# Kernel optimization log

Hardware: AMD Instinct MI355X
Metric: run time of the kernel (lower is better)

## Reference

```python
import jax, jax.numpy as jnp
import numpy as np

N = 4096
DIM = 128      # dim_in
HID = 256      # mlp hidden_dim
K_IN = 8       # k for linear_k

def _knn_edges(dist, k):
    # dist: [n,n]; k nearest neighbors excluding self (matches heapq loop)
    n = dist.shape[0]
    d = jnp.where(jnp.eye(n, dtype=bool), jnp.inf, dist)
    nbr = jax.lax.top_k(-d, k)[1]                     # [n,k] indices of k smallest
    src = jnp.repeat(jnp.arange(n), k)                # res[0] = i
    dst = nbr.reshape(-1)                             # res[1] = neighbor
    return src, dst

def _gcn_conv(x, src, dst, W, b):
    # torch_geometric GCNConv: add self loops + symmetric normalization
    n = x.shape[0]
    loop = jnp.arange(n)
    s = jnp.concatenate([src, loop])
    t = jnp.concatenate([dst, loop])
    xw = x @ W
    deg = jax.ops.segment_sum(jnp.ones(s.shape[0], x.dtype), t, num_segments=n)
    dinv = jax.lax.rsqrt(deg)                         # deg >= 1 due to self loops
    norm = dinv[s] * dinv[t]
    out = jax.ops.segment_sum(norm[:, None] * xw[s], t, num_segments=n)
    return out + b

def _gcn(x, src, dst, Wg1, bg1, Wg2, bg2):
    h = jax.nn.relu(_gcn_conv(x, src, dst, Wg1, bg1))
    h = _gcn_conv(h, src, dst, Wg2, bg2)              # dropout is identity in eval
    return jax.nn.log_softmax(h, axis=1)

def _conv2d(x, w, b):
    y = jax.lax.conv_general_dilated(x, w, (1, 1), 'SAME',
        dimension_numbers=('NCHW', 'OIHW', 'NCHW'))
    return y + b.reshape(1, -1, 1, 1)

def setup_inputs():
    key = jax.random.key(0)
    ks = jax.random.split(key, 20)
    f32 = jnp.float32
    def w(k, shape):
        fan = shape[0]
        return (jax.random.uniform(k, shape, f32) * 2 - 1) * (1.0 / np.sqrt(fan))
    return {
        'data_x_1': jax.random.normal(ks[0], (1, N, 4), f32),
        'data_x_2': jax.random.normal(ks[1], (1, N, K_IN, 4), f32),
        'Wk': w(ks[2], (K_IN, 1)),        'bk': jnp.zeros((1,), f32),
        'Wg1': w(ks[3], (8, DIM // 2)),   'bg1': jnp.zeros((DIM // 2,), f32),
        'Wg2': w(ks[4], (DIM // 2, DIM)), 'bg2': jnp.zeros((DIM,), f32),
        'Wq': w(ks[5], (3 * DIM, DIM)),   'bq': jnp.zeros((DIM,), f32),
        'Wkey': w(ks[6], (3 * DIM, DIM)), 'bkey': jnp.zeros((DIM,), f32),
        'Woff': w(ks[7], (4, DIM)),       'boff': jnp.zeros((DIM,), f32),
        'pw': jnp.full((1,), 0.25, f32),
        'Wf1': w(ks[8], (DIM, HID)),      'bf1': jnp.zeros((HID,), f32),
        'Wf2': w(ks[9], (HID, HID)),      'bf2': jnp.zeros((HID,), f32),
        'Wf3': w(ks[10], (HID, 4)),       'bf3': jnp.zeros((4,), f32),
        'Wcy3': w(ks[11], (1, 1, 1, 3)),  'bcy3': jnp.zeros((1,), f32),
        'Wcx3': w(ks[12], (1, 1, 3, 1)),  'bcx3': jnp.zeros((1,), f32),
        'Wcy5': w(ks[13], (1, 1, 1, 5)),  'bcy5': jnp.zeros((1,), f32),
        'Wcx5': w(ks[14], (1, 1, 5, 1)),  'bcx5': jnp.zeros((1,), f32),
        'Wcy9': w(ks[15], (1, 1, 1, 9)),  'bcy9': jnp.zeros((1,), f32),
        'Wcx9': w(ks[16], (1, 1, 9, 1)),  'bcx9': jnp.zeros((1,), f32),
    }

def reference(data_x_1, data_x_2, Wk, bk, Wg1, bg1, Wg2, bg2, Wq, bq, Wkey, bkey,
              Woff, boff, pw, Wf1, bf1, Wf2, bf2, Wf3, bf3,
              Wcy3, bcy3, Wcx3, bcx3, Wcy5, bcy5, Wcx5, bcx5, Wcy9, bcy9, Wcx9, bcx9):
    # linear_k over k dimension: [1,n,k,4] -> transpose -> [1,n,4,k] -> [1,n,4]
    dx2 = jnp.swapaxes(data_x_2, 2, 3)
    dx2_out = (dx2 @ Wk + bk)[..., 0]
    data_x = jnp.concatenate([data_x_1, dx2_out], axis=2)   # [1,n,8]
    Ot = data_x[:, :, 4:]                                   # [1,n,4]

    pos = data_x[:, :, 0:2]
    diff = pos[:, :, None, :] - pos[:, None, :, :]          # [1,n,n,2]
    distances = jnp.linalg.norm(diff, axis=3)               # [1,n,n]
    maxd = jnp.max(distances, axis=2, keepdims=True)
    oushi_atte = 1.0 - distances / maxd                     # [1,n,n]

    x0 = data_x[0]
    dist0 = jax.lax.stop_gradient(distances[0])             # knn on detached dist
    embs = []
    for kk in (3, 5, 9):
        src, dst = _knn_edges(dist0, kk)
        embs.append(_gcn(x0, src, dst, Wg1, bg1, Wg2, bg2)[None])
    embedding = jnp.concatenate(embs, axis=2)               # [1,n,3*DIM]

    query = embedding @ Wq + bq                             # [1,n,DIM]
    key_t = embedding @ Wkey + bkey
    scores = jnp.einsum('bnd,bmd->bnm', query, key_t) / jnp.sqrt(jnp.float32(DIM))
    A = scores / jnp.max(scores, axis=2, keepdims=True)     # [1,n,n]

    A4 = A[None]                                            # [1,1,n,n]
    c3 = _conv2d(A4, Wcy3, bcy3) + _conv2d(A4, Wcx3, bcx3)
    c5 = _conv2d(A4, Wcy5, bcy5) + _conv2d(A4, Wcx5, bcx5)
    c9 = _conv2d(A4, Wcy9, bcy9) + _conv2d(A4, Wcx9, bcx9)

    A_cat = jnp.concatenate([A, oushi_atte, c3[0], c5[0], c9[0]], axis=2)  # [1,n,5n]
    A_cat = (A_cat - A_cat.min()) / (A_cat.max() - A_cat.min())

    Ot5 = jnp.tile(Ot, (1, 5, 1))                           # [1,5n,4]
    h = jnp.matmul(A_cat, Ot5)                              # [1,n,4]
    h = h @ Woff + boff                                     # [1,n,DIM]
    h = jnp.where(h > 0, h, pw * h)                         # PReLU (scalar weight)
    h = jax.nn.relu(h @ Wf1 + bf1)
    h = jax.nn.relu(h @ Wf2 + bf2)
    return h @ Wf3 + bf3                                    # [1,n,4]
```

## Files before the change

kernel.cpp:

```cpp
#include <hip/hip_runtime.h>
#include <math.h>

#define NN 4096

static __device__ __forceinline__ unsigned enc_f(float f){
    unsigned u = __float_as_uint(f);
    return (u & 0x80000000u) ? ~u : (u | 0x80000000u);
}
static __device__ __forceinline__ float dec_f(unsigned u){
    unsigned b = (u & 0x80000000u) ? (u & 0x7fffffffu) : ~u;
    return __uint_as_float(b);
}

__global__ void k_prep(const float* __restrict__ dx1, const float* __restrict__ dx2,
                       const float* __restrict__ Wk, const float* __restrict__ bk,
                       float* __restrict__ x0, float* __restrict__ colsum){
    int n = blockIdx.x*blockDim.x + threadIdx.x;
    if (n >= NN) return;
    float wk[8];
    #pragma unroll
    for (int j=0;j<8;j++) wk[j] = Wk[j];
    float bkv = bk[0];
    #pragma unroll
    for (int c=0;c<4;c++) x0[n*8+c] = dx1[n*4+c];
    #pragma unroll
    for (int c=0;c<4;c++){
        float acc = bkv;
        #pragma unroll
        for (int j=0;j<8;j++) acc += dx2[(n*8+j)*4+c]*wk[j];
        x0[n*8+4+c] = acc;
        atomicAdd(&colsum[c], acc);
    }
}

__global__ __launch_bounds__(256) void k_dist(const float* __restrict__ dx1,
        float* __restrict__ maxd, int* __restrict__ nbr,
        int* __restrict__ cnt3, int* __restrict__ cnt5, int* __restrict__ cnt9){
    __shared__ float2 ps[NN];
    int tid = threadIdx.x;
    for (int j=tid; j<NN; j+=256){
        float4 v = *(const float4*)&dx1[j*4];
        ps[j] = make_float2(v.x, v.y);
    }
    __syncthreads();
    int lane = tid & 63;
    int i = blockIdx.x*4 + (tid>>6);
    float2 pi = ps[i];
    unsigned long long best[9];
    #pragma unroll
    for (int q=0;q<9;q++) best[q] = ~0ULL;
    float lmax = 0.f;
    for (int t=0;t<64;t++){
        int j = (t<<6) | lane;
        float2 p = ps[j];
        float dx = pi.x - p.x, dy = pi.y - p.y;
        float d = sqrtf(dx*dx + dy*dy);
        lmax = fmaxf(lmax, d);
        unsigned long long cand = ((unsigned long long)__float_as_uint(d) << 32) | (unsigned)j;
        if (j != i && cand < best[8]){
            best[8] = cand;
            #pragma unroll
            for (int q=8; q>0; --q){
                if (best[q] < best[q-1]){ unsigned long long tm=best[q]; best[q]=best[q-1]; best[q-1]=tm; }
            }
        }
    }
    #pragma unroll
    for (int m=1;m<64;m<<=1) lmax = fmaxf(lmax, __shfl_xor(lmax, m, 64));
    if (lane==0) maxd[i] = lmax;
    for (int t=0;t<9;t++){
        unsigned long long w = best[0];
        #pragma unroll
        for (int m=1;m<64;m<<=1){
            unsigned long long o = __shfl_xor(w, m, 64);
            if (o < w) w = o;
        }
        if (best[0] == w){
            #pragma unroll
            for (int q=0;q<8;q++) best[q] = best[q+1];
            best[8] = ~0ULL;
        }
        if (lane==0){
            int j = (int)(w & 0xffffffffu);
            nbr[i*9+t] = j;
            atomicAdd(&cnt9[j], 1);
            if (t<5) atomicAdd(&cnt5[j], 1);
            if (t<3) atomicAdd(&cnt3[j], 1);
        }
    }
}

__global__ __launch_bounds__(256) void k_scan(const int* __restrict__ cnt3,
        const int* __restrict__ cnt5, const int* __restrict__ cnt9,
        int* __restrict__ offc, float* __restrict__ dinvc){
    __shared__ int part[256];
    int tid = threadIdx.x;
    for (int g=0; g<3; g++){
        const int* cp = g==0?cnt3:(g==1?cnt5:cnt9);
        int base = tid*16;
        int loc[16]; int s=0;
        #pragma unroll
        for (int q=0;q<16;q++){ loc[q]=s; s += cp[base+q]; }
        part[tid]=s; __syncthreads();
        for (int d=1; d<256; d<<=1){
            int v = (tid>=d) ? part[tid-d] : 0;
            __syncthreads();
            part[tid] += v;
            __syncthreads();
        }
        int pre = (tid==0) ? 0 : part[tid-1];
        #pragma unroll
        for (int q=0;q<16;q++){
            offc[g*NN + base + q]  = pre + loc[q];
            dinvc[g*NN + base + q] = rsqrtf((float)cp[base+q] + 1.f);
        }
        __syncthreads();
    }
}

__global__ void k_fill(const int* __restrict__ nbr, const int* __restrict__ offc,
        int* __restrict__ cur, int* __restrict__ rev){
    int i = blockIdx.x*256 + threadIdx.x;
    if (i >= NN) return;
    #pragma unroll
    for (int t=0;t<9;t++){
        int j = nbr[i*9+t];
        int gmin = t<3 ? 0 : (t<5 ? 1 : 2);
        for (int g=gmin; g<3; g++){
            int pos = atomicAdd(&cur[g*NN+j], 1);
            int rb = (g==0) ? 0 : (g==1 ? NN*3 : NN*8);
            rev[rb + offc[g*NN+j] + pos] = i;
        }
    }
}

__global__ void k_y1(const float* __restrict__ x0, const float* __restrict__ Wg1,
                     float* __restrict__ xw){
    int idx = blockIdx.x*256 + threadIdx.x;
    if (idx >= NN*64) return;
    int n = idx>>6, c = idx&63;
    float acc = 0.f;
    #pragma unroll
    for (int k=0;k<8;k++) acc += x0[n*8+k]*Wg1[k*64+c];
    xw[idx] = acc;
}

__global__ __launch_bounds__(256) void k_h1y2(const float* __restrict__ xw,
        const int* __restrict__ offc,
        const int* __restrict__ cnt3, const int* __restrict__ cnt5, const int* __restrict__ cnt9,
        const int* __restrict__ rev, const float* __restrict__ dinvc,
        const float* __restrict__ bg1, const float* __restrict__ Wg2,
        float* __restrict__ y2){
    __shared__ float h1s[12][64];
    int n0 = blockIdx.x*4, tid = threadIdx.x;
    for (int s=tid; s<768; s+=256){
        int p = s>>6, k = s&63, g = p>>2, n = n0+(p&3);
        const int* cp = g==0?cnt3:(g==1?cnt5:cnt9);
        int rb = (g==0) ? 0 : (g==1 ? NN*3 : NN*8);
        int cnt = cp[n];
        int o = rb + offc[g*NN+n];
        float dv = dinvc[g*NN+n];
        float srow = dv*xw[n*64+k];
        for (int e=0;e<cnt;e++){
            int i = rev[o+e];
            srow += dinvc[g*NN+i]*xw[i*64+k];
        }
        float v = dv*srow + bg1[k];
        h1s[p][k] = v>0.f ? v : 0.f;
    }
    __syncthreads();
    int c = tid & 127, ph = tid>>7;
    float a6[6] = {0,0,0,0,0,0};
    for (int k=0;k<64;k++){
        float w = Wg2[k*128+c];
        #pragma unroll
        for (int q=0;q<6;q++) a6[q] += h1s[q*2+ph][k]*w;
    }
    #pragma unroll
    for (int q=0;q<6;q++){
        int p = q*2+ph, g = p>>2, n = n0+(p&3);
        float dv = dinvc[g*NN+n];
        y2[(size_t)g*NN*128 + (size_t)n*128 + c] = dv*a6[q];
    }
}

__global__ __launch_bounds__(128) void k_fin(const float* __restrict__ y2,
        const int* __restrict__ offc,
        const int* __restrict__ cnt3, const int* __restrict__ cnt5, const int* __restrict__ cnt9,
        const int* __restrict__ rev, const float* __restrict__ dinvc,
        const float* __restrict__ bg2, float* __restrict__ emb){
    __shared__ float sm[2], ss[2];
    int b = blockIdx.x;
    int n = b & (NN-1), g = b >> 12;
    const int* cp = g==0?cnt3:(g==1?cnt5:cnt9);
    int rb = (g==0) ? 0 : (g==1 ? NN*3 : NN*8);
    int cnt = cp[n];
    int o = rb + offc[g*NN+n];
    float dv = dinvc[g*NN+n];
    int c = threadIdx.x;
    const float* yg = y2 + (size_t)g*NN*128;
    float s = yg[(size_t)n*128 + c];
    for (int e=0;e<cnt;e++){
        int i = rev[o+e];
        s += yg[(size_t)i*128 + c];
    }
    float v = dv*s + bg2[c];
    float m = v;
    #pragma unroll
    for (int st=1;st<64;st<<=1) m = fmaxf(m, __shfl_xor(m, st, 64));
    if ((c&63)==0) sm[c>>6] = m;
    __syncthreads();
    m = fmaxf(sm[0], sm[1]);
    float e = expf(v - m);
    float t = e;
    #pragma unroll
    for (int st=1;st<64;st<<=1) t += __shfl_xor(t, st, 64);
    if ((c&63)==0) ss[c>>6] = t;
    __syncthreads();
    t = ss[0]+ss[1];
    emb[n*384 + g*128 + c] = v - m - logf(t);
}

__global__ __launch_bounds__(256) void k_qk(const float* __restrict__ emb,
        const float* __restrict__ Wq, const float* __restrict__ bq,
        const float* __restrict__ Wkey, const float* __restrict__ bkey,
        float* __restrict__ q, float* __restrict__ kbuf){
    __shared__ float es[8][384];
    int n0 = blockIdx.x*8;
    int tid = threadIdx.x;
    for (int idx=tid; idx<8*384; idx+=256){
        int m = idx/384, k = idx%384;
        es[m][k] = emb[(n0+m)*384+k];
    }
    __syncthreads();
    int c = tid & 127;
    int sel = tid >> 7;
    const float* W = sel ? Wkey : Wq;
    float b = sel ? bkey[c] : bq[c];
    float acc[8];
    #pragma unroll
    for (int m=0;m<8;m++) acc[m]=b;
    for (int k=0;k<384;k++){
        float w = W[k*128+c];
        #pragma unroll
        for (int m=0;m<8;m++) acc[m] += es[m][k]*w;
    }
    float* out = sel ? kbuf : q;
    #pragma unroll
    for (int m=0;m<8;m++) out[(n0+m)*128+c] = acc[m];
}

__global__ __launch_bounds__(256) void k_scores(const float* __restrict__ q,
        const float* __restrict__ kb, float* __restrict__ scores,
        unsigned* __restrict__ rowmaxenc){
    __shared__ float at[32][132];
    __shared__ float bt[32][132];
    int bx = blockIdx.x & 31;
    int by = blockIdx.x >> 5;
    int r0 = by*128, c0 = bx*128;
    int tid = threadIdx.x;
    int tx = tid & 15, ty = tid >> 4;
    float acc[8][8] = {};
    for (int k0 = 0; k0 < 128; k0 += 32){
        __syncthreads();
        #pragma unroll
        for (int l=0; l<4; l++){
            int idx = tid + l*256;
            int rowi = idx >> 3;
            int kq  = (idx & 7) * 4;
            float4 a = *(const float4*)&q [(size_t)(r0+rowi)*128 + k0 + kq];
            float4 b = *(const float4*)&kb[(size_t)(c0+rowi)*128 + k0 + kq];
            at[kq+0][rowi]=a.x; at[kq+1][rowi]=a.y; at[kq+2][rowi]=a.z; at[kq+3][rowi]=a.w;
            bt[kq+0][rowi]=b.x; bt[kq+1][rowi]=b.y; bt[kq+2][rowi]=b.z; bt[kq+3][rowi]=b.w;
        }
        __syncthreads();
        #pragma unroll
        for (int k=0;k<32;k++){
            float4 a0 = *(const float4*)&at[k][ty*4];
            float4 a1 = *(const float4*)&at[k][64+ty*4];
            float4 b0 = *(const float4*)&bt[k][tx*4];
            float4 b1 = *(const float4*)&bt[k][64+tx*4];
            float av[8] = {a0.x,a0.y,a0.z,a0.w,a1.x,a1.y,a1.z,a1.w};
            float bv[8] = {b0.x,b0.y,b0.z,b0.w,b1.x,b1.y,b1.z,b1.w};
            #pragma unroll
            for (int u=0;u<8;u++){
                #pragma unroll
                for (int v=0;v<8;v++) acc[u][v] += av[u]*bv[v];
            }
        }
    }
    #pragma unroll
    for (int u=0;u<8;u++){
        int rr = r0 + ((u<4)? ty*4+u : 64+ty*4+(u-4));
        float4 s0 = {acc[u][0],acc[u][1],acc[u][2],acc[u][3]};
        float4 s1 = {acc[u][4],acc[u][5],acc[u][6],acc[u][7]};
        *(float4*)&scores[(size_t)rr*NN + c0 + tx*4] = s0;
        *(float4*)&scores[(size_t)rr*NN + c0 + 64 + tx*4] = s1;
        float m = acc[u][0];
        #pragma unroll
        for (int v=1;v<8;v++) m = fmaxf(m, acc[u][v]);
        #pragma unroll
        for (int s=1;s<16;s<<=1) m = fmaxf(m, __shfl_xor(m, s, 64));
        if (tx==0) atomicMax(&rowmaxenc[rr], enc_f(m));
    }
}

__global__ __launch_bounds__(256) void k_mcat(const float* __restrict__ scores,
        const unsigned* __restrict__ rowmaxenc, const float* __restrict__ maxd,
        const float* __restrict__ dx1, const float* __restrict__ x0,
        const float* __restrict__ Wcy3, const float* __restrict__ Wcx3,
        const float* __restrict__ Wcy5, const float* __restrict__ Wcx5,
        const float* __restrict__ Wcy9, const float* __restrict__ Wcx9,
        const float* __restrict__ bcy3, const float* __restrict__ bcx3,
        const float* __restrict__ bcy5, const float* __restrict__ bcx5,
        const float* __restrict__ bcy9, const float* __restrict__ bcx9,
        float* __restrict__ mnmx, float* __restrict__ hpart){
    __shared__ float As[40][76];
    __shared__ float invr[40];
    __shared__ float2 pj[64];
    __shared__ float4 ots[64];
    __shared__ float2 pi[32];
    __shared__ float im[32];
    __shared__ float smn[256], smx[256];
    int xb = blockIdx.x, yb = blockIdx.y;
    int i0 = yb*32, j0 = xb*64;
    int tid = threadIdx.x;
    float wy3[3],wx3[3],wy5[5],wx5[5],wy9[9],wx9[9];
    #pragma unroll
    for (int t=0;t<3;t++){ wy3[t]=Wcy3[t]; wx3[t]=Wcx3[t]; }
    #pragma unroll
    for (int t=0;t<5;t++){ wy5[t]=Wcy5[t]; wx5[t]=Wcx5[t]; }
    #pragma unroll
    for (int t=0;t<9;t++){ wy9[t]=Wcy9[t]; wx9[t]=Wcx9[t]; }
    float bc3 = bcy3[0]+bcx3[0];
    float bc5 = bcy5[0]+bcx5[0];
    float bc9 = bcy9[0]+bcx9[0];
    if (tid < 40){
        int gr = i0-4+tid;
        invr[tid] = ((unsigned)gr < NN) ? 1.f/dec_f(rowmaxenc[gr]) : 0.f;
    } else if (tid >= 64 && tid < 128){
        int c = tid-64, j = j0+c;
        float4 v = *(const float4*)&dx1[j*4];
        pj[c] = make_float2(v.x, v.y);
        ots[c] = *(const float4*)&x0[j*8+4];
    } else if (tid >= 128 && tid < 160){
        int r = tid-128;
        float4 v = *(const float4*)&dx1[(i0+r)*4];
        pi[r] = make_float2(v.x, v.y);
        im[r] = 1.f/maxd[i0+r];
    }
    __syncthreads();
    for (int idx=tid; idx<40*72; idx+=256){
        int lr = idx/72, lc = idx - lr*72;
        int gr = i0-4+lr, gc = j0-4+lc;
        float v = 0.f;
        if ((unsigned)gr < NN && (unsigned)gc < NN)
            v = scores[(size_t)gr*NN + gc]*invr[lr];
        As[lr][lc] = v;
    }
    __syncthreads();
    int r = tid>>3, cb = tid&7, c0l = cb*8;
    float acc9[8]={0,0,0,0,0,0,0,0}, acc5[8]={0,0,0,0,0,0,0,0}, acc3[8]={0,0,0,0,0,0,0,0}, ctr[8];
    #pragma unroll
    for (int u=0;u<9;u++){
        float4 a = *(const float4*)&As[r+u][c0l+4];
        float4 b = *(const float4*)&As[r+u][c0l+8];
        float vals[8] = {a.x,a.y,a.z,a.w,b.x,b.y,b.z,b.w};
        #pragma unroll
        for (int q=0;q<8;q++){
            acc9[q] += vals[q]*wx9[u];
            if (u>=2 && u<=6) acc5[q] += vals[q]*wx5[u-2];
            if (u>=3 && u<=5) acc3[q] += vals[q]*wx3[u-3];
            if (u==4) ctr[q] = vals[q];
        }
    }
    float win[16];
    #pragma unroll
    for (int q4=0;q4<4;q4++){
        float4 w4 = *(const float4*)&As[r+4][c0l+q4*4];
        win[q4*4+0]=w4.x; win[q4*4+1]=w4.y; win[q4*4+2]=w4.z; win[q4*4+3]=w4.w;
    }
    float mn = INFINITY, mx = -INFINITY;
    float pd0=0,pd1=0,pd2=0,pd3=0;
    float2 ppi = pi[r];
    float imv = im[r];
    #pragma unroll
    for (int q=0;q<8;q++){
        float cy9=0.f;
        #pragma unroll
        for (int u=0;u<9;u++) cy9 += win[q+u]*wy9[u];
        float cy5=0.f;
        #pragma unroll
        for (int u=0;u<5;u++) cy5 += win[q+2+u]*wy5[u];
        float cy3=0.f;
        #pragma unroll
        for (int u=0;u<3;u++) cy3 += win[q+3+u]*wy3[u];
        float c3v = cy3+acc3[q]+bc3;
        float c5v = cy5+acc5[q]+bc5;
        float c9v = cy9+acc9[q]+bc9;
        float a = ctr[q];
        float2 pjv = pj[c0l+q];
        float dxp = ppi.x-pjv.x, dyp = ppi.y-pjv.y;
        float ou = 1.f - sqrtf(dxp*dxp+dyp*dyp)*imv;
        float Mv = a + ou + c3v + c5v + c9v;
        mn = fminf(mn, fminf(fminf(a,ou), fminf(fminf(c3v,c5v),c9v)));
        mx = fmaxf(mx, fmaxf(fmaxf(a,ou), fmaxf(fmaxf(c3v,c5v),c9v)));
        float4 ot = ots[c0l+q];
        pd0 += Mv*ot.x; pd1 += Mv*ot.y; pd2 += Mv*ot.z; pd3 += Mv*ot.w;
    }
    #pragma unroll
    for (int m=1;m<8;m<<=1){
        pd0 += __shfl_xor(pd0, m, 64);
        pd1 += __shfl_xor(pd1, m, 64);
        pd2 += __shfl_xor(pd2, m, 64);
        pd3 += __shfl_xor(pd3, m, 64);
    }
    if (cb==0){
        float4 pd = {pd0,pd1,pd2,pd3};
        *(float4*)&hpart[((size_t)(i0+r)*64 + xb)*4] = pd;
    }
    smn[tid]=mn; smx[tid]=mx; __syncthreads();
    for (int s=128;s>0;s>>=1){
        if (tid<s){ smn[tid]=fminf(smn[tid],smn[tid+s]); smx[tid]=fmaxf(smx[tid],smx[tid+s]); }
        __syncthreads();
    }
    if (tid==0){
        int bid = yb*64 + xb;
        mnmx[bid] = smn[0];
        mnmx[8192 + bid] = smx[0];
    }
}

__global__ __launch_bounds__(256) void k_gmm(const float* __restrict__ mnmx, float* __restrict__ gmm){
    __shared__ float smn[256], smx[256];
    int tid = threadIdx.x;
    float mn = INFINITY, mx = -INFINITY;
    for (int i=tid; i<8192; i+=256){
        mn = fminf(mn, mnmx[i]);
        mx = fmaxf(mx, mnmx[8192+i]);
    }
    smn[tid]=mn; smx[tid]=mx; __syncthreads();
    for (int s=128;s>0;s>>=1){
        if (tid<s){ smn[tid]=fminf(smn[tid],smn[tid+s]); smx[tid]=fmaxf(smx[tid],smx[tid+s]); }
        __syncthreads();
    }
    if (tid==0){ gmm[0]=smn[0]; gmm[1]=smx[0]; }
}

__global__ __launch_bounds__(256) void k_hred(const float* __restrict__ hpart,
        const float* __restrict__ gmm, const float* __restrict__ colsum,
        float* __restrict__ hfin){
    int i = blockIdx.x*256 + threadIdx.x;
    if (i >= NN) return;
    float4 sum = {0,0,0,0};
    const float4* hp = (const float4*)hpart + (size_t)i*64;
    for (int xb=0; xb<64; xb++){
        float4 v = hp[xb];
        sum.x+=v.x; sum.y+=v.y; sum.z+=v.z; sum.w+=v.w;
    }
    float mnv = gmm[0], mxv = gmm[1];
    float s = 1.f/(mxv-mnv), o = -mnv*s;
    float4 cs = *(const float4*)colsum;
    float4 out;
    out.x = s*sum.x + 5.f*o*cs.x;
    out.y = s*sum.y + 5.f*o*cs.y;
    out.z = s*sum.z + 5.f*o*cs.z;
    out.w = s*sum.w + 5.f*o*cs.w;
    *(float4*)&hfin[i*4] = out;
}

__global__ __launch_bounds__(256) void k_mlp(const float* __restrict__ hfin,
        const float* __restrict__ Woff, const float* __restrict__ boff, const float* __restrict__ pw,
        const float* __restrict__ Wf1, const float* __restrict__ bf1,
        const float* __restrict__ Wf2, const float* __restrict__ bf2,
        const float* __restrict__ Wf3, const float* __restrict__ bf3,
        float* __restrict__ out){
    __shared__ float h1[8][128];
    __shared__ float h2[8][256];
    __shared__ float h3[8][256];
    __shared__ float4 red4[256];
    int n0 = blockIdx.x*8, tid = threadIdx.x;
    float p = pw[0];
    {
        int c = tid & 127, mb = (tid>>7)*4;
        #pragma unroll
        for (int mm=0; mm<4; mm++){
            int m = mb+mm;
            float v = boff[c];
            #pragma unroll
            for (int k=0;k<4;k++) v += hfin[(n0+m)*4+k]*Woff[k*128+c];
            h1[m][c] = v>0.f ? v : p*v;
        }
    }
    __syncthreads();
    {
        int c = tid;
        float acc[8];
        #pragma unroll
        for (int m=0;m<8;m++) acc[m] = bf1[c];
        for (int k=0;k<128;k++){
            float w = Wf1[k*256+c];
            #pragma unroll
            for (int m=0;m<8;m++) acc[m] += h1[m][k]*w;
        }
        #pragma unroll
        for (int m=0;m<8;m++) h2[m][c] = acc[m]>0.f?acc[m]:0.f;
    }
    __syncthreads();
    {
        int c = tid;
        float acc[8];
        #pragma unroll
        for (int m=0;m<8;m++) acc[m] = bf2[c];
        for (int k=0;k<256;k++){
            float w = Wf2[k*256+c];
            #pragma unroll
            for (int m=0;m<8;m++) acc[m] += h2[m][k]*w;
        }
        #pragma unroll
        for (int m=0;m<8;m++) h3[m][c] = acc[m]>0.f?acc[m]:0.f;
    }
    __syncthreads();
    float w3_0 = Wf3[tid*4+0], w3_1 = Wf3[tid*4+1], w3_2 = Wf3[tid*4+2], w3_3 = Wf3[tid*4+3];
    for (int m=0;m<8;m++){
        float hv = h3[m][tid];
        float4 r; r.x = hv*w3_0; r.y = hv*w3_1; r.z = hv*w3_2; r.w = hv*w3_3;
        red4[tid]=r; __syncthreads();
        for (int s=128;s>0;s>>=1){
            if(tid<s){
                red4[tid].x+=red4[tid+s].x; red4[tid].y+=red4[tid+s].y;
                red4[tid].z+=red4[tid+s].z; red4[tid].w+=red4[tid+s].w;
            }
            __syncthreads();
        }
        if (tid==0){
            float4 o;
            o.x = red4[0].x + bf3[0]; o.y = red4[0].y + bf3[1];
            o.z = red4[0].z + bf3[2]; o.w = red4[0].w + bf3[3];
            *(float4*)&out[(n0+m)*4] = o;
        }
        __syncthreads();
    }
}

extern "C" void kernel_launch(void* const* d_in, const int* in_sizes, int n_in,
                              void* d_out, int out_size, void* d_ws, size_t ws_size,
                              hipStream_t stream){
    const float* dx1  = (const float*)d_in[0];
    const float* dx2  = (const float*)d_in[1];
    const float* Wk   = (const float*)d_in[2];
    const float* bk   = (const float*)d_in[3];
    const float* Wg1  = (const float*)d_in[4];
    const float* bg1  = (const float*)d_in[5];
    const float* Wg2  = (const float*)d_in[6];
    const float* bg2  = (const float*)d_in[7];
    const float* Wq   = (const float*)d_in[8];
    const float* bq   = (const float*)d_in[9];
    const float* Wkey = (const float*)d_in[10];
    const float* bkey = (const float*)d_in[11];
    const float* Woff = (const float*)d_in[12];
    const float* boff = (const float*)d_in[13];
    const float* pw   = (const float*)d_in[14];
    const float* Wf1  = (const float*)d_in[15];
    const float* bf1  = (const float*)d_in[16];
    const float* Wf2  = (const float*)d_in[17];
    const float* bf2  = (const float*)d_in[18];
    const float* Wf3  = (const float*)d_in[19];
    const float* bf3  = (const float*)d_in[20];
    const float* Wcy3 = (const float*)d_in[21];
    const float* bcy3 = (const float*)d_in[22];
    const float* Wcx3 = (const float*)d_in[23];
    const float* bcx3 = (const float*)d_in[24];
    const float* Wcy5 = (const float*)d_in[25];
    const float* bcy5 = (const float*)d_in[26];
    const float* Wcx5 = (const float*)d_in[27];
    const float* bcx5 = (const float*)d_in[28];
    const float* Wcy9 = (const float*)d_in[29];
    const float* bcy9 = (const float*)d_in[30];
    const float* Wcx9 = (const float*)d_in[31];
    const float* bcx9 = (const float*)d_in[32];

    char* ws = (char*)d_ws;
    size_t off = 0;
    auto alloc = [&](size_t b)->void*{ void* p = ws + off; off += (b + 255) & ~(size_t)255; return p; };

    char* zbase = ws + off;
    float*    colsum    = (float*)   alloc(4*4);
    int*      cnt3      = (int*)     alloc((size_t)NN*4);
    int*      cnt5      = (int*)     alloc((size_t)NN*4);
    int*      cnt9      = (int*)     alloc((size_t)NN*4);
    int*      cur       = (int*)     alloc((size_t)3*NN*4);
    unsigned* rowmaxenc = (unsigned*)alloc((size_t)NN*4);
    size_t zbytes = (size_t)((ws + off) - zbase);

    float* x0     = (float*)alloc((size_t)NN*8*4);
    float* maxd   = (float*)alloc((size_t)NN*4);
    int*   nbr    = (int*)  alloc((size_t)NN*9*4);
    int*   offc   = (int*)  alloc((size_t)3*NN*4);
    float* dinvc  = (float*)alloc((size_t)3*NN*4);
    int*   rev    = (int*)  alloc((size_t)NN*17*4);
    float* xw     = (float*)alloc((size_t)NN*64*4);
    float* y2     = (float*)alloc((size_t)3*NN*128*4);
    float* emb    = (float*)alloc((size_t)NN*384*4);
    float* qb     = (float*)alloc((size_t)NN*128*4);
    float* kb     = (float*)alloc((size_t)NN*128*4);
    float* scores = (float*)alloc((size_t)NN*NN*4);
    float* mnmx   = (float*)alloc((size_t)2*8192*4);
    float* hpart  = (float*)alloc((size_t)NN*64*4*4);
    float* gmm    = (float*)alloc(2*4);
    float* hfin   = (float*)alloc((size_t)NN*4*4);
    (void)ws_size; (void)in_sizes; (void)n_in; (void)out_size;

    hipMemsetAsync(zbase, 0, zbytes, stream);

    k_prep<<<16,256,0,stream>>>(dx1,dx2,Wk,bk,x0,colsum);
    k_dist<<<NN/4,256,0,stream>>>(dx1,maxd,nbr,cnt3,cnt5,cnt9);
    k_scan<<<1,256,0,stream>>>(cnt3,cnt5,cnt9,offc,dinvc);
    k_fill<<<16,256,0,stream>>>(nbr,offc,cur,rev);

    k_y1  <<<NN*64/256,256,0,stream>>>(x0,Wg1,xw);
    k_h1y2<<<NN/4,256,0,stream>>>(xw,offc,cnt3,cnt5,cnt9,rev,dinvc,bg1,Wg2,y2);
    k_fin <<<NN*3,128,0,stream>>>(y2,offc,cnt3,cnt5,cnt9,rev,dinvc,bg2,emb);

    k_qk<<<NN/8,256,0,stream>>>(emb,Wq,bq,Wkey,bkey,qb,kb);
    k_scores<<<1024,256,0,stream>>>(qb,kb,scores,rowmaxenc);
    k_mcat<<<dim3(64,128),256,0,stream>>>(scores,rowmaxenc,maxd,dx1,x0,
        Wcy3,Wcx3,Wcy5,Wcx5,Wcy9,Wcx9,
        bcy3,bcx3,bcy5,bcx5,bcy9,bcx9, mnmx, hpart);
    k_gmm<<<1,256,0,stream>>>(mnmx,gmm);
    k_hred<<<NN/256,256,0,stream>>>(hpart,gmm,colsum,hfin);
    k_mlp<<<NN/8,256,0,stream>>>(hfin,Woff,boff,pw,Wf1,bf1,Wf2,bf2,Wf3,bf3,(float*)d_out);
}
```

Measured before the change: 354.7 us.

## Enlarge mcat tiles, vectorize swizzled score loads, move A min/max into scores

The fused conv/concat kernel now works on 64x64 tiles instead of 32x64. This cuts the share of halo rows re-read from the large scores matrix. Tiles are loaded as float4 into an XOR-swizzled shared-memory layout, each thread computes two output rows, and the block min/max uses wave shuffles instead of a 256-entry shared tree. The per-row min of the scores is now gathered with atomics in the scores kernel, so the global normalization bounds for A and the oushi term come from row min/max (oushi assumed to span [0,1]). This costs an extra atomicMin per row segment and an extra memset.

```diff
diff --git a/kernel.cpp b/kernel.cpp
--- a/kernel.cpp
+++ b/kernel.cpp
@@ -252,7 +252,7 @@
 
 __global__ __launch_bounds__(256) void k_scores(const float* __restrict__ q,
         const float* __restrict__ kb, float* __restrict__ scores,
-        unsigned* __restrict__ rowmaxenc){
+        unsigned* __restrict__ rowmaxenc, unsigned* __restrict__ rowminenc){
     __shared__ float at[32][132];
     __shared__ float bt[32][132];
     int bx = blockIdx.x & 31;
@@ -296,12 +296,18 @@
         float4 s1 = {acc[u][4],acc[u][5],acc[u][6],acc[u][7]};
         *(float4*)&scores[(size_t)rr*NN + c0 + tx*4] = s0;
         *(float4*)&scores[(size_t)rr*NN + c0 + 64 + tx*4] = s1;
-        float m = acc[u][0];
-        #pragma unroll
-        for (int v=1;v<8;v++) m = fmaxf(m, acc[u][v]);
-        #pragma unroll
-        for (int s=1;s<16;s<<=1) m = fmaxf(m, __shfl_xor(m, s, 64));
-        if (tx==0) atomicMax(&rowmaxenc[rr], enc_f(m));
+        float m = acc[u][0], mn = acc[u][0];
+        #pragma unroll
+        for (int v=1;v<8;v++){ m = fmaxf(m, acc[u][v]); mn = fminf(mn, acc[u][v]); }
+        #pragma unroll
+        for (int s=1;s<16;s<<=1){
+            m  = fmaxf(m,  __shfl_xor(m,  s, 64));
+            mn = fminf(mn, __shfl_xor(mn, s, 64));
+        }
+        if (tx==0){
+            atomicMax(&rowmaxenc[rr], enc_f(m));
+            atomicMin(&rowminenc[rr], enc_f(mn));
+        }
     }
 }
 
@@ -315,16 +321,17 @@
         const float* __restrict__ bcy5, const float* __restrict__ bcx5,
         const float* __restrict__ bcy9, const float* __restrict__ bcx9,
         float* __restrict__ mnmx, float* __restrict__ hpart){
-    __shared__ float As[40][76];
-    __shared__ float invr[40];
-    __shared__ float2 pj[64];
+    __shared__ float As[72][96];
+    __shared__ float invr_s[72];
     __shared__ float4 ots[64];
-    __shared__ float2 pi[32];
-    __shared__ float im[32];
-    __shared__ float smn[256], smx[256];
-    int xb = blockIdx.x, yb = blockIdx.y;
-    int i0 = yb*32, j0 = xb*64;
+    __shared__ float2 pjv[64];
+    __shared__ float2 piv[64];
+    __shared__ float ims[64];
+    __shared__ float smn[4], smx[4];
+    int bx = blockIdx.x, by = blockIdx.y;
+    int i0 = by*64, j0 = bx*64;
     int tid = threadIdx.x;
+
     float wy3[3],wx3[3],wy5[5],wx5[5],wy9[9],wx9[9];
     #pragma unroll
     for (int t=0;t<3;t++){ wy3[t]=Wcy3[t]; wx3[t]=Wcx3[t]; }
@@ -335,109 +342,157 @@
     float bc3 = bcy3[0]+bcx3[0];
     float bc5 = bcy5[0]+bcx5[0];
     float bc9 = bcy9[0]+bcx9[0];
-    if (tid < 40){
+
+    if (tid < 72){
         int gr = i0-4+tid;
-        invr[tid] = ((unsigned)gr < NN) ? 1.f/dec_f(rowmaxenc[gr]) : 0.f;
-    } else if (tid >= 64 && tid < 128){
-        int c = tid-64, j = j0+c;
+        invr_s[tid] = ((unsigned)gr < NN) ? 1.f/dec_f(rowmaxenc[gr]) : 0.f;
+    } else if (tid >= 96 && tid < 160){
+        int c = tid-96, j = j0+c;
         float4 v = *(const float4*)&dx1[j*4];
-        pj[c] = make_float2(v.x, v.y);
+        pjv[c] = make_float2(v.x, v.y);
         ots[c] = *(const float4*)&x0[j*8+4];
-    } else if (tid >= 128 && tid < 160){
-        int r = tid-128;
+    } else if (tid >= 160 && tid < 224){
+        int r = tid-160;
         float4 v = *(const float4*)&dx1[(i0+r)*4];
-        pi[r] = make_float2(v.x, v.y);
-        im[r] = 1.f/maxd[i0+r];
-    }
-    __syncthreads();
-    for (int idx=tid; idx<40*72; idx+=256){
-        int lr = idx/72, lc = idx - lr*72;
-        int gr = i0-4+lr, gc = j0-4+lc;
-        float v = 0.f;
-        if ((unsigned)gr < NN && (unsigned)gc < NN)
-            v = scores[(size_t)gr*NN + gc]*invr[lr];
-        As[lr][lc] = v;
-    }
-    __syncthreads();
-    int r = tid>>3, cb = tid&7, c0l = cb*8;
-    float acc9[8]={0,0,0,0,0,0,0,0}, acc5[8]={0,0,0,0,0,0,0,0}, acc3[8]={0,0,0,0,0,0,0,0}, ctr[8];
-    #pragma unroll
-    for (int u=0;u<9;u++){
-        float4 a = *(const float4*)&As[r+u][c0l+4];
-        float4 b = *(const float4*)&As[r+u][c0l+8];
-        float vals[8] = {a.x,a.y,a.z,a.w,b.x,b.y,b.z,b.w};
-        #pragma unroll
-        for (int q=0;q<8;q++){
-            acc9[q] += vals[q]*wx9[u];
-            if (u>=2 && u<=6) acc5[q] += vals[q]*wx5[u-2];
-            if (u>=3 && u<=5) acc3[q] += vals[q]*wx3[u-3];
-            if (u==4) ctr[q] = vals[q];
-        }
-    }
-    float win[16];
-    #pragma unroll
-    for (int q4=0;q4<4;q4++){
-        float4 w4 = *(const float4*)&As[r+4][c0l+q4*4];
-        win[q4*4+0]=w4.x; win[q4*4+1]=w4.y; win[q4*4+2]=w4.z; win[q4*4+3]=w4.w;
-    }
+        piv[r] = make_float2(v.x, v.y);
+        ims[r] = 1.f/maxd[i0+r];
+    }
+    __syncthreads();
+
+    bool colEdge = (bx == 0) || (bx == 63);
+    for (int s = tid; s < 72*20; s += 256){
+        int row = s/20, c4 = s - row*20;
+        int gr = i0 - 4 + row;
+        int grc = gr < 0 ? 0 : (gr > NN-1 ? NN-1 : gr);
+        int gcf = j0 - 8 + c4*4;
+        float iv = invr_s[row];
+        float4 v;
+        if (!colEdge){
+            v = *(const float4*)&scores[(size_t)grc*NN + gcf];
+        } else {
+            v = make_float4(0.f,0.f,0.f,0.f);
+            const float* rp = &scores[(size_t)grc*NN];
+            if ((unsigned)(gcf+0) < NN) v.x = rp[gcf+0];
+            if ((unsigned)(gcf+1) < NN) v.y = rp[gcf+1];
+            if ((unsigned)(gcf+2) < NN) v.z = rp[gcf+2];
+            if ((unsigned)(gcf+3) < NN) v.w = rp[gcf+3];
+        }
+        int sc4 = c4 ^ ((row & 3) << 1);
+        float* dst = &As[row][sc4*4];
+        dst[0]=v.x*iv; dst[1]=v.y*iv; dst[2]=v.z*iv; dst[3]=v.w*iv;
+    }
+    __syncthreads();
+
+    int rp = tid >> 3, cg = tid & 7;
+    int r0l = rp*2;
     float mn = INFINITY, mx = -INFINITY;
-    float pd0=0,pd1=0,pd2=0,pd3=0;
-    float2 ppi = pi[r];
-    float imv = im[r];
-    #pragma unroll
-    for (int q=0;q<8;q++){
-        float cy9=0.f;
-        #pragma unroll
-        for (int u=0;u<9;u++) cy9 += win[q+u]*wy9[u];
-        float cy5=0.f;
-        #pragma unroll
-        for (int u=0;u<5;u++) cy5 += win[q+2+u]*wy5[u];
-        float cy3=0.f;
-        #pragma unroll
-        for (int u=0;u<3;u++) cy3 += win[q+3+u]*wy3[u];
-        float c3v = cy3+acc3[q]+bc3;
-        float c5v = cy5+acc5[q]+bc5;
-        float c9v = cy9+acc9[q]+bc9;
-        float a = ctr[q];
-        float2 pjv = pj[c0l+q];
-        float dxp = ppi.x-pjv.x, dyp = ppi.y-pjv.y;
-        float ou = 1.f - sqrtf(dxp*dxp+dyp*dyp)*imv;
-        float Mv = a + ou + c3v + c5v + c9v;
-        mn = fminf(mn, fminf(fminf(a,ou), fminf(fminf(c3v,c5v),c9v)));
-        mx = fmaxf(mx, fmaxf(fmaxf(a,ou), fmaxf(fmaxf(c3v,c5v),c9v)));
-        float4 ot = ots[c0l+q];
-        pd0 += Mv*ot.x; pd1 += Mv*ot.y; pd2 += Mv*ot.z; pd3 += Mv*ot.w;
-    }
-    #pragma unroll
-    for (int m=1;m<8;m<<=1){
-        pd0 += __shfl_xor(pd0, m, 64);
-        pd1 += __shfl_xor(pd1, m, 64);
-        pd2 += __shfl_xor(pd2, m, 64);
-        pd3 += __shfl_xor(pd3, m, 64);
-    }
-    if (cb==0){
-        float4 pd = {pd0,pd1,pd2,pd3};
-        *(float4*)&hpart[((size_t)(i0+r)*64 + xb)*4] = pd;
-    }
-    smn[tid]=mn; smx[tid]=mx; __syncthreads();
-    for (int s=128;s>0;s>>=1){
-        if (tid<s){ smn[tid]=fminf(smn[tid],smn[tid+s]); smx[tid]=fmaxf(smx[tid],smx[tid+s]); }
-        __syncthreads();
-    }
-    if (tid==0){
-        int bid = yb*64 + xb;
-        mnmx[bid] = smn[0];
-        mnmx[8192 + bid] = smx[0];
-    }
-}
-
-__global__ __launch_bounds__(256) void k_gmm(const float* __restrict__ mnmx, float* __restrict__ gmm){
+    float pdx[2]={0,0}, pdy[2]={0,0}, pdz[2]={0,0}, pdw[2]={0,0};
+    float2 prow0 = piv[r0l], prow1 = piv[r0l+1];
+    float im0 = ims[r0l], im1 = ims[r0l+1];
+
+    for (int h = 0; h < 2; ++h){
+        int cbase = cg*8 + h*4;
+        float colw[10][4];
+        #pragma unroll
+        for (int u=0; u<10; ++u){
+            int row = r0l+u;
+            int c4 = ((cbase+8)>>2) ^ ((row&3)<<1);
+            float4 v = *(const float4*)&As[row][c4*4];
+            colw[u][0]=v.x; colw[u][1]=v.y; colw[u][2]=v.z; colw[u][3]=v.w;
+        }
+        #pragma unroll
+        for (int d=0; d<2; ++d){
+            int row = r0l+4+d;
+            float w[12];
+            {
+                int c4l = ((cbase+4)>>2) ^ ((row&3)<<1);
+                int c4r = ((cbase+12)>>2) ^ ((row&3)<<1);
+                float4 l = *(const float4*)&As[row][c4l*4];
+                float4 rgt = *(const float4*)&As[row][c4r*4];
+                w[0]=l.x; w[1]=l.y; w[2]=l.z; w[3]=l.w;
+                #pragma unroll
+                for (int k=0;k<4;++k) w[4+k] = colw[4+d][k];
+                w[8]=rgt.x; w[9]=rgt.y; w[10]=rgt.z; w[11]=rgt.w;
+            }
+            float2 prow = d ? prow1 : prow0;
+            float imv = d ? im1 : im0;
+            #pragma unroll
+            for (int c=0;c<4;++c){
+                float cx9 = 0.f, cx5 = 0.f, cx3 = 0.f;
+                #pragma unroll
+                for (int u=0;u<9;++u) cx9 += colw[u+d][c]*wx9[u];
+                #pragma unroll
+                for (int u=0;u<5;++u) cx5 += colw[u+2+d][c]*wx5[u];
+                #pragma unroll
+                for (int u=0;u<3;++u) cx3 += colw[u+3+d][c]*wx3[u];
+                float cy9 = bc9, cy5 = bc5, cy3 = bc3;
+                #pragma unroll
+                for (int u=0;u<9;++u) cy9 += w[c+u]*wy9[u];
+                #pragma unroll
+                for (int u=0;u<5;++u) cy5 += w[c+2+u]*wy5[u];
+                #pragma unroll
+                for (int u=0;u<3;++u) cy3 += w[c+3+u]*wy3[u];
+                float c3v = cy3+cx3, c5v = cy5+cx5, c9v = cy9+cx9;
+                mn = fminf(mn, fminf(fminf(c3v,c5v),c9v));
+                mx = fmaxf(mx, fmaxf(fmaxf(c3v,c5v),c9v));
+                float a = colw[4+d][c];
+                float2 pj2 = pjv[cbase+c];
+                float ddx = prow.x - pj2.x, ddy = prow.y - pj2.y;
+                float ou = 1.f - sqrtf(ddx*ddx + ddy*ddy)*imv;
+                float Mv = a + ou + c3v + c5v + c9v;
+                float4 ot = ots[cbase+c];
+                if (d==0){ pdx[0]+=Mv*ot.x; pdy[0]+=Mv*ot.y; pdz[0]+=Mv*ot.z; pdw[0]+=Mv*ot.w; }
+                else     { pdx[1]+=Mv*ot.x; pdy[1]+=Mv*ot.y; pdz[1]+=Mv*ot.z; pdw[1]+=Mv*ot.w; }
+            }
+        }
+    }
+    #pragma unroll
+    for (int m=1; m<8; m<<=1){
+        #pragma unroll
+        for (int d=0; d<2; ++d){
+            pdx[d] += __shfl_xor(pdx[d], m, 64);
+            pdy[d] += __shfl_xor(pdy[d], m, 64);
+            pdz[d] += __shfl_xor(pdz[d], m, 64);
+            pdw[d] += __shfl_xor(pdw[d], m, 64);
+        }
+    }
+    if (cg == 0){
+        #pragma unroll
+        for (int d=0; d<2; ++d){
+            float4 pd = {pdx[d], pdy[d], pdz[d], pdw[d]};
+            *(float4*)&hpart[((size_t)(i0 + r0l + d)*64 + bx)*4] = pd;
+        }
+    }
+    #pragma unroll
+    for (int m=1; m<64; m<<=1){
+        mn = fminf(mn, __shfl_xor(mn, m, 64));
+        mx = fmaxf(mx, __shfl_xor(mx, m, 64));
+    }
+    int wid = tid >> 6;
+    if ((tid & 63) == 0){ smn[wid] = mn; smx[wid] = mx; }
+    __syncthreads();
+    if (tid == 0){
+        float a0 = fminf(fminf(smn[0],smn[1]), fminf(smn[2],smn[3]));
+        float b0 = fmaxf(fmaxf(smx[0],smx[1]), fmaxf(smx[2],smx[3]));
+        int bid = by*64 + bx;
+        mnmx[bid] = a0;
+        mnmx[4096 + bid] = b0;
+    }
+}
+
+__global__ __launch_bounds__(256) void k_gmm(const float* __restrict__ mnmx,
+        const unsigned* __restrict__ rowminenc, const unsigned* __restrict__ rowmaxenc,
+        float* __restrict__ gmm){
     __shared__ float smn[256], smx[256];
     int tid = threadIdx.x;
-    float mn = INFINITY, mx = -INFINITY;
-    for (int i=tid; i<8192; i+=256){
+    float mn = 0.f, mx = 1.f;
+    for (int i=tid; i<4096; i+=256){
         mn = fminf(mn, mnmx[i]);
-        mx = fmaxf(mx, mnmx[8192+i]);
+        mx = fmaxf(mx, mnmx[4096+i]);
+        float rmx = dec_f(rowmaxenc[i]);
+        float q = dec_f(rowminenc[i]) / rmx;
+        mn = fminf(mn, fminf(1.f, q));
+        mx = fmaxf(mx, fmaxf(1.f, q));
     }
     smn[tid]=mn; smx[tid]=mx; __syncthreads();
     for (int s=128;s>0;s>>=1){
@@ -592,6 +647,7 @@
     int*      cur       = (int*)     alloc((size_t)3*NN*4);
     unsigned* rowmaxenc = (unsigned*)alloc((size_t)NN*4);
     size_t zbytes = (size_t)((ws + off) - zbase);
+    unsigned* rowminenc = (unsigned*)alloc((size_t)NN*4);
 
     float* x0     = (float*)alloc((size_t)NN*8*4);
     float* maxd   = (float*)alloc((size_t)NN*4);
@@ -605,13 +661,14 @@
     float* qb     = (float*)alloc((size_t)NN*128*4);
     float* kb     = (float*)alloc((size_t)NN*128*4);
     float* scores = (float*)alloc((size_t)NN*NN*4);
-    float* mnmx   = (float*)alloc((size_t)2*8192*4);
+    float* mnmx   = (float*)alloc((size_t)2*4096*4);
     float* hpart  = (float*)alloc((size_t)NN*64*4*4);
     float* gmm    = (float*)alloc(2*4);
     float* hfin   = (float*)alloc((size_t)NN*4*4);
     (void)ws_size; (void)in_sizes; (void)n_in; (void)out_size;
 
     hipMemsetAsync(zbase, 0, zbytes, stream);
+    hipMemsetAsync(rowminenc, 0xFF, (size_t)NN*4, stream);
 
     k_prep<<<16,256,0,stream>>>(dx1,dx2,Wk,bk,x0,colsum);
     k_dist<<<NN/4,256,0,stream>>>(dx1,maxd,nbr,cnt3,cnt5,cnt9);
@@ -623,11 +680,11 @@
     k_fin <<<NN*3,128,0,stream>>>(y2,offc,cnt3,cnt5,cnt9,rev,dinvc,bg2,emb);
 
     k_qk<<<NN/8,256,0,stream>>>(emb,Wq,bq,Wkey,bkey,qb,kb);
-    k_scores<<<1024,256,0,stream>>>(qb,kb,scores,rowmaxenc);
-    k_mcat<<<dim3(64,128),256,0,stream>>>(scores,rowmaxenc,maxd,dx1,x0,
+    k_scores<<<1024,256,0,stream>>>(qb,kb,scores,rowmaxenc,rowminenc);
+    k_mcat<<<dim3(64,64),256,0,stream>>>(scores,rowmaxenc,maxd,dx1,x0,
         Wcy3,Wcx3,Wcy5,Wcx5,Wcy9,Wcx9,
         bcy3,bcx3,bcy5,bcx5,bcy9,bcx9, mnmx, hpart);
-    k_gmm<<<1,256,0,stream>>>(mnmx,gmm);
+    k_gmm<<<1,256,0,stream>>>(mnmx,rowminenc,rowmaxenc,gmm);
     k_hred<<<NN/256,256,0,stream>>>(hpart,gmm,colsum,hfin);
     k_mlp<<<NN/8,256,0,stream>>>(hfin,Woff,boff,pw,Wf1,bf1,Wf2,bf2,Wf3,bf3,(float*)d_out);
 }
```

Result: faster. 335.0 us (-5.5%).
